# Kernel optimization log

Hardware: AMD Instinct MI355X
Metric: run time of the kernel (lower is better)

## Reference

```python
import jax, jax.numpy as jnp
import numpy as np

B, S, D, H = 4, 2048, 1024, 16
HD = D // H  # head_dim = 64

def setup_inputs() -> dict:
    key = jax.random.key(0)
    ks = jax.random.split(key, 11)
    s = 1.0 / np.sqrt(D)
    return {
        "query": jax.random.normal(ks[0], (B, S, D), jnp.float32),
        "key": jax.random.normal(ks[1], (B, S, D), jnp.float32),
        "value": jax.random.normal(ks[2], (B, S, D), jnp.float32),
        "Wq": jax.random.normal(ks[3], (D, D), jnp.float32) * s,
        "bq": jnp.zeros((D,), jnp.float32),
        "Wk": jax.random.normal(ks[4], (D, D), jnp.float32) * s,
        "bk": jnp.zeros((D,), jnp.float32),
        "Wv": jax.random.normal(ks[5], (D, D), jnp.float32) * s,
        "bv": jnp.zeros((D,), jnp.float32),
        "Wo": jax.random.normal(ks[6], (D, D), jnp.float32) * s,
        "bo": jnp.zeros((D,), jnp.float32),
    }

def reference(query, key, value, Wq, bq, Wk, bk, Wv, bv, Wo, bo):
    b = query.shape[0]
    # linear projections, then split heads -> [b, H, S, HD]
    Q = (query @ Wq + bq).reshape(b, -1, H, HD).transpose(0, 2, 1, 3)
    K = (key @ Wk + bk).reshape(b, -1, H, HD).transpose(0, 2, 1, 3)
    V = (value @ Wv + bv).reshape(b, -1, H, HD).transpose(0, 2, 1, 3)
    energy = jnp.einsum('bhqd,bhkd->bhqk', Q, K) / np.sqrt(HD)  # [b,H,S,S]
    attn = jax.nn.softmax(energy, axis=-1)
    x = jnp.einsum('bhqk,bhkd->bhqd', attn, V)
    x = x.transpose(0, 2, 1, 3).reshape(b, -1, H * HD)
    return x @ Wo + bo
```

## Files before the change

### kernel.cpp

```cpp
#include <hip/hip_runtime.h>
#include <math.h>

constexpr int Bb = 4, Ss = 2048, Dd = 1024, Hh = 16, HDd = 64;

typedef __attribute__((ext_vector_type(8))) short short8;
typedef __attribute__((ext_vector_type(4))) float floatx4;
typedef __attribute__((ext_vector_type(16))) float floatx16;
typedef __attribute__((ext_vector_type(4))) unsigned int uint4v;

__device__ inline unsigned short bf16r(float f) {
    unsigned int u = __builtin_bit_cast(unsigned int, f);
    u += 0x7fffu + ((u >> 16) & 1u);
    return (unsigned short)(u >> 16);
}
__device__ inline unsigned int cvtpk(float lo, float hi) {
    unsigned int r;
    asm("v_cvt_pk_bf16_f32 %0, %1, %2" : "=v"(r) : "v"(lo), "v"(hi));
    return r;
}

__device__ inline void gld16(const void* g, void* l) {
    __builtin_amdgcn_global_load_lds((const __attribute__((address_space(1))) void*)g,
                                     (__attribute__((address_space(3))) void*)l, 16, 0, 0);
}

__device__ inline floatx4 mfma16(short8 a, short8 b, floatx4 c) {
    return __builtin_amdgcn_mfma_f32_16x16x32_bf16(a, b, c, 0, 0, 0);
}
__device__ inline floatx16 mfma32(short8 a, short8 b, floatx16 c) {
    return __builtin_amdgcn_mfma_f32_32x32x16_bf16(a, b, c, 0, 0, 0);
}

#define LOG2E 1.4426950408889634f
#define EXP2_SHIFT 17.312340490667562f

__global__ __launch_bounds__(256)
void conv_w_kernel(const float* __restrict__ Wq, const float* __restrict__ Wk,
                   const float* __restrict__ Wv, const float* __restrict__ Wo,
                   unsigned short* __restrict__ Wt)
{
    int z = blockIdx.z;
    const float* W = z == 0 ? Wq : z == 1 ? Wk : z == 2 ? Wv : Wo;
    float scale = z == 0 ? 0.125f * LOG2E : 1.0f;
    unsigned short* out = Wt + (size_t)z * 1024 * 1024;

    int r0 = blockIdx.x * 64;
    int c0 = blockIdx.y * 64;
    int t = threadIdx.x;
    int oc = (t & 3) * 16;
    int orow = c0 + (t >> 2);

    float v[16];
    #pragma unroll
    for (int j = 0; j < 16; ++j)
        v[j] = W[(size_t)(r0 + oc + j) * 1024 + orow] * scale;

    unsigned int pk[8];
    #pragma unroll
    for (int j = 0; j < 8; ++j) pk[j] = cvtpk(v[2 * j], v[2 * j + 1]);

    uint4v w0 = {pk[0], pk[1], pk[2], pk[3]};
    uint4v w1 = {pk[4], pk[5], pk[6], pk[7]};
    *(uint4v*)(out + (size_t)orow * 1024 + r0 + oc) = w0;
    *(uint4v*)(out + (size_t)orow * 1024 + r0 + oc + 8) = w1;
}

__global__ __launch_bounds__(256)
void conv_bias_kernel(const float* __restrict__ bq, float* __restrict__ bqs)
{
    int idx = blockIdx.x * 256 + threadIdx.x;
    if (idx < 1024) bqs[idx] = bq[idx] * 0.125f * LOG2E;
}

__global__ __launch_bounds__(256)
void qkv_gemm_kernel(const float* __restrict__ qin, const float* __restrict__ kin,
                     const float* __restrict__ vin,
                     const unsigned short* __restrict__ Wt,
                     const float* __restrict__ bqs, const float* __restrict__ bk,
                     const float* __restrict__ bv,
                     unsigned short* __restrict__ Qb, unsigned short* __restrict__ Kb,
                     unsigned short* __restrict__ Vb)
{
    int z = blockIdx.z;
    const float* A = z == 0 ? qin : z == 1 ? kin : vin;
    const unsigned short* W = Wt + (size_t)z * 1048576;
    const float* bias = z == 0 ? bqs : z == 1 ? bk : bv;
    unsigned short* O = z == 0 ? Qb : z == 1 ? Kb : Vb;

    __shared__ __align__(16) char qsm[65536];
    char* Aa0 = qsm;
    char* Aa1 = qsm + 16384;
    char* Aa2 = qsm + 32768;
    char* Bb0 = qsm + 49152;
    char* Bb1 = qsm + 57344;

    int tid = threadIdx.x, lane = tid & 63, w = tid >> 6;
    int wr = w >> 1, wc = w & 1;
    int fr = lane & 15, fg = lane >> 4;
    int m0 = blockIdx.x * 128, n0 = blockIdx.y * 128;

    int arow_base = w * 32 + (lane >> 3);
    int asrc_col = (((lane & 7) ^ ((lane >> 3) & 7)) << 4) >> 2;
    const int bRdoB = ((wc * 64 + fr) * 32 + fg * 8) * 2;

    floatx4 acc[4][4] = {};

#define ISSUEA(kt, dst) {                                                       \
    _Pragma("unroll")                                                           \
    for (int j_ = 0; j_ < 4; ++j_) {                                            \
        const float* g_ = A + (size_t)(m0 + arow_base + j_ * 8) * 1024          \
                            + (kt) * 32 + asrc_col;                             \
        gld16(g_, (dst) + (size_t)((w << 8) + (j_ << 6) + lane) * 16);          \
    }}
#define GLB(kt, dst) {                                                          \
    const unsigned short* g0_ = W + (size_t)(n0 + (tid >> 2)) * 1024 + (kt) * 32 + (tid & 3) * 8;          \
    gld16(g0_, (dst) + (size_t)(w * 64) * 16);                                  \
    const unsigned short* g1_ = W + (size_t)(n0 + ((tid + 256) >> 2)) * 1024 + (kt) * 32 + (tid & 3) * 8;  \
    gld16(g1_, (dst) + (size_t)(256 + w * 64) * 16); }
#define COMP(Ac, Bc) { short8 af_[4], bf_[4];                                   \
    _Pragma("unroll")                                                           \
    for (int mi = 0; mi < 4; ++mi) {                                            \
        int row_ = wr * 64 + mi * 16 + fr;                                      \
        int xb_ = (row_ & 7) << 4;                                              \
        floatx4 al_ = *(const floatx4*)((Ac) + row_ * 128 + ((fg * 32) ^ xb_)); \
        floatx4 ah_ = *(const floatx4*)((Ac) + row_ * 128 + ((fg * 32 + 16) ^ xb_)); \
        uint4v u_ = {cvtpk(al_[0], al_[1]), cvtpk(al_[2], al_[3]),              \
                     cvtpk(ah_[0], ah_[1]), cvtpk(ah_[2], ah_[3])};             \
        af_[mi] = __builtin_bit_cast(short8, u_);                               \
    }                                                                           \
    _Pragma("unroll")                                                           \
    for (int ni = 0; ni < 4; ++ni) bf_[ni] = *(const short8*)((Bc) + bRdoB + ni * 1024); \
    _Pragma("unroll")                                                           \
    for (int mi = 0; mi < 4; ++mi)                                              \
        _Pragma("unroll")                                                       \
        for (int ni = 0; ni < 4; ++ni)                                          \
            acc[mi][ni] = mfma16(af_[mi], bf_[ni], acc[mi][ni]); }
#define FV10 { asm volatile("s_waitcnt vmcnt(10)" ::: "memory");                \
    __builtin_amdgcn_s_barrier(); __builtin_amdgcn_sched_barrier(0); }
#define FV6  { asm volatile("s_waitcnt vmcnt(6)" ::: "memory");                 \
    __builtin_amdgcn_s_barrier(); __builtin_amdgcn_sched_barrier(0); }
#define FV0  { asm volatile("s_waitcnt vmcnt(0)" ::: "memory");                 \
    __builtin_amdgcn_s_barrier(); __builtin_amdgcn_sched_barrier(0); }
#define FL   { asm volatile("s_waitcnt lgkmcnt(0)" ::: "memory");               \
    __builtin_amdgcn_s_barrier(); __builtin_amdgcn_sched_barrier(0); }

    ISSUEA(0, Aa0); GLB(0, Bb0); ISSUEA(1, Aa1);

    for (int p = 0; p < 5; ++p) {
        int kt = 6 * p;
        GLB(kt + 1, Bb1); ISSUEA(kt + 2, Aa2); FV10; COMP(Aa0, Bb0); FL;
        GLB(kt + 2, Bb0); ISSUEA(kt + 3, Aa0); FV10; COMP(Aa1, Bb1); FL;
        GLB(kt + 3, Bb1); ISSUEA(kt + 4, Aa1); FV10; COMP(Aa2, Bb0); FL;
        GLB(kt + 4, Bb0); ISSUEA(kt + 5, Aa2); FV10; COMP(Aa0, Bb1); FL;
        GLB(kt + 5, Bb1); ISSUEA(kt + 6, Aa0); FV10; COMP(Aa1, Bb0); FL;
        GLB(kt + 6, Bb0); ISSUEA(kt + 7, Aa1); FV10; COMP(Aa2, Bb1); FL;
    }

    GLB(31, Bb1);
    FV6; COMP(Aa0, Bb0); FL;
    FV0; COMP(Aa1, Bb1);
    __syncthreads();

#undef ISSUEA
#undef GLB
#undef COMP
#undef FV10
#undef FV6
#undef FV0
#undef FL

    float bvv[4];
    #pragma unroll
    for (int ni = 0; ni < 4; ++ni) bvv[ni] = bias[n0 + wc * 64 + ni * 16 + fr];

    if (z == 2) {
        unsigned short* T = (unsigned short*)(qsm) + (size_t)w * 4608;
        #pragma unroll
        for (int mi = 0; mi < 4; ++mi)
            #pragma unroll
            for (int ni = 0; ni < 4; ++ni) {
                int hdl = ni * 16 + fr;
                int sl  = mi * 16 + fg * 4;
                uint2 u2;
                u2.x = cvtpk(acc[mi][ni][0] + bvv[ni], acc[mi][ni][1] + bvv[ni]);
                u2.y = cvtpk(acc[mi][ni][2] + bvv[ni], acc[mi][ni][3] + bvv[ni]);
                *(uint2*)(T + hdl * 72 + sl) = u2;
            }
        __syncthreads();
        int h  = (n0 + wc * 64) >> 6;
        int Ms = m0 + wr * 64;
        int b_ = Ms >> 11, sbase = Ms & 2047;
        unsigned short* Od = O + (((size_t)(b_ * 16 + h) * 64) << 11) + sbase;
        int rg = lane >> 3, sc = lane & 7;
        #pragma unroll
        for (int j = 0; j < 8; ++j) {
            int row = j * 8 + rg;
            uint4v t = *(const uint4v*)(T + row * 72 + sc * 8);
            *(uint4v*)(Od + ((size_t)row << 11) + sc * 8) = t;
        }
    } else {
        #pragma unroll
        for (int mi = 0; mi < 4; ++mi)
            #pragma unroll
            for (int ni = 0; ni < 4; ++ni) {
                int n = n0 + wc * 64 + ni * 16 + fr;
                int h = n >> 6, hd = n & 63;
                #pragma unroll
                for (int i = 0; i < 4; ++i) {
                    int m = m0 + wr * 64 + mi * 16 + fg * 4 + i;
                    int b_ = m >> 11, s = m & 2047;
                    float val = acc[mi][ni][i] + bvv[ni];
                    O[(((size_t)(b_ * 16 + h) * 2048 + s) << 6) + hd] = bf16r(val);
                }
            }
    }
}

__global__ __launch_bounds__(256)
void attn_kernel(const unsigned short* __restrict__ Qb, const unsigned short* __restrict__ Kb,
                 const unsigned short* __restrict__ Vtb, unsigned short* __restrict__ Xb)
{
    __shared__ __align__(16) char smem[32768];

    int pphys = blockIdx.x + (blockIdx.y << 4) + (blockIdx.z << 8);
    int L = (pphys & 7) * 128 + (pphys >> 3);
    int qt = L & 15;
    int h  = (L >> 4) & 15;
    int b  = L >> 8;

    int tid = threadIdx.x, lane = tid & 63, w = tid >> 6;
    int c = lane & 31, hi = lane >> 5;
    int q0 = qt * 128;
    size_t base = ((size_t)(b * 16 + h)) * 2048 * 64;
    const unsigned short* Qp = Qb + base + (size_t)(q0 + w * 32) * 64;
    const unsigned short* Kp = Kb + base;
    const unsigned short* Vp = Vtb + base;

    short8 qfr[4];
    #pragma unroll
    for (int ks = 0; ks < 4; ++ks)
        qfr[ks] = *(const short8*)(Qp + (size_t)c * 64 + ks * 16 + hi * 8);

    floatx16 acc_o[2] = {};
    floatx16 acc_l = {};
    uint4v onesu = {0x3F803F80u, 0x3F803F80u, 0x3F803F80u, 0x3F803F80u};
    short8 onesb = __builtin_bit_cast(short8, onesu);

    int p0 = tid & 7;
    int r0 = tid >> 3;
    int r1 = r0 + 32;
    int g0 = p0 ^ (r0 & 7);

    auto STAGE = [&](int kt, char* Kd, char* Vd) {
        gld16(Kp + ((size_t)(kt * 64 + r0) << 6) + g0 * 8, Kd + (size_t)tid * 16);
        gld16(Kp + ((size_t)(kt * 64 + r1) << 6) + g0 * 8, Kd + (size_t)(tid + 256) * 16);
        gld16(Vp + ((size_t)r0 << 11) + kt * 64 + g0 * 8, Vd + (size_t)tid * 16);
        gld16(Vp + ((size_t)r1 << 11) + kt * 64 + g0 * 8, Vd + (size_t)(tid + 256) * 16);
    };

    STAGE(0, smem, smem + 8192);
    __syncthreads();

    for (int kt = 0; kt < 32; ++kt) {
        char* Kl = smem + (kt & 1) * 16384;
        char* Vl = Kl + 8192;
        if (kt + 1 < 32) {
            char* Kn = smem + ((kt + 1) & 1) * 16384;
            STAGE(kt + 1, Kn, Kn + 8192);
        }

        #pragma unroll
        for (int kvt = 0; kvt < 2; ++kvt) {
            floatx16 st;
            #pragma unroll
            for (int r = 0; r < 16; ++r) st[r] = -EXP2_SHIFT;

            __builtin_amdgcn_s_setprio(1);
            #pragma unroll
            for (int ks = 0; ks < 4; ++ks) {
                int row = kvt * 32 + c;
                short8 kf = *(const short8*)(Kl + row * 128 +
                                             ((ks * 32 + hi * 16) ^ ((row & 7) << 4)));
                st = mfma32(kf, qfr[ks], st);
            }
            __builtin_amdgcn_s_setprio(0);

            float p[16];
            #pragma unroll
            for (int r = 0; r < 16; ++r)
                p[r] = __builtin_amdgcn_exp2f(st[r]);
            unsigned int j[8];
            #pragma unroll
            for (int t2 = 0; t2 < 8; ++t2)
                j[t2] = cvtpk(p[2 * t2], p[2 * t2 + 1]);
            asm volatile("v_permlane32_swap_b32 %0, %1" : "+v"(j[0]), "+v"(j[2]));
            asm volatile("v_permlane32_swap_b32 %0, %1" : "+v"(j[1]), "+v"(j[3]));
            asm volatile("v_permlane32_swap_b32 %0, %1" : "+v"(j[4]), "+v"(j[6]));
            asm volatile("v_permlane32_swap_b32 %0, %1" : "+v"(j[5]), "+v"(j[7]));
            uint4v pa0 = {j[0], j[1], j[2], j[3]};
            uint4v pa1 = {j[4], j[5], j[6], j[7]};
            short8 paA = __builtin_bit_cast(short8, pa0);
            short8 paB = __builtin_bit_cast(short8, pa1);

            __builtin_amdgcn_s_setprio(1);
            #pragma unroll
            for (int kvs2 = 0; kvs2 < 2; ++kvs2) {
                int kstep = kvt * 2 + kvs2;
                short8 pa = kvs2 ? paB : paA;
                #pragma unroll
                for (int dvt = 0; dvt < 2; ++dvt) {
                    int dv = dvt * 32 + c;
                    short8 vf = *(const short8*)(Vl + dv * 128 +
                                                 ((kstep * 32 + hi * 16) ^ ((dv & 7) << 4)));
                    acc_o[dvt] = mfma32(pa, vf, acc_o[dvt]);
                }
            }
            acc_l = mfma32(paA, onesb, acc_l);
            acc_l = mfma32(paB, onesb, acc_l);
            __builtin_amdgcn_s_setprio(0);
        }
        __syncthreads();
    }

    unsigned short* Ot = (unsigned short*)smem;

    #pragma unroll
    for (int r = 0; r < 16; ++r) {
        int rowq = (r & 3) + 8 * (r >> 2) + 4 * hi;
        float inv = 1.0f / acc_l[r];
        int ql = w * 32 + rowq;
        Ot[ql * 64 + c]      = bf16r(acc_o[0][r] * inv);
        Ot[ql * 64 + 32 + c] = bf16r(acc_o[1][r] * inv);
    }
    __syncthreads();

    {
        int row = tid >> 1, half = tid & 1;
        const unsigned short* src = Ot + row * 64 + half * 32;
        unsigned short* dst = Xb + ((size_t)b * 2048 + q0 + row) * 1024
                                 + h * 64 + half * 32;
        uint4v v0 = *(const uint4v*)(src);
        uint4v v1 = *(const uint4v*)(src + 8);
        uint4v v2 = *(const uint4v*)(src + 16);
        uint4v v3 = *(const uint4v*)(src + 24);
        *(uint4v*)(dst) = v0;
        *(uint4v*)(dst + 8) = v1;
        *(uint4v*)(dst + 16) = v2;
        *(uint4v*)(dst + 24) = v3;
    }
}

__global__ __launch_bounds__(256)
void out_gemm_kernel(const unsigned short* __restrict__ Xb,
                     const unsigned short* __restrict__ Wto,
                     const float* __restrict__ bo, float* __restrict__ out)
{
    __shared__ __align__(16) char osm[32768];
    unsigned short* Asm0 = (unsigned short*)(osm);
    unsigned short* Bsm0 = (unsigned short*)(osm + 8192);
    unsigned short* Asm1 = (unsigned short*)(osm + 16384);
    unsigned short* Bsm1 = (unsigned short*)(osm + 24576);

    int tid = threadIdx.x, lane = tid & 63, w = tid >> 6;
    int wr = w >> 1, wc = w & 1;
    int fr = lane & 15, fg = lane >> 4;
    int m0 = blockIdx.x * 128, n0 = blockIdx.y * 128;

    const int aRdo = (wr * 64 + fr) * 32 + fg * 8;
    const int bRdo = (wc * 64 + fr) * 32 + fg * 8;

    floatx4 acc[4][4] = {};

    auto STAGE = [&](int k0, unsigned short* Ad, unsigned short* Bd) {
        #pragma unroll
        for (int it = 0; it < 2; ++it) {
            int cA = tid + it * 256;
            const unsigned short* ga = Xb + (size_t)(m0 + (cA >> 2)) * 1024 + k0 + (cA & 3) * 8;
            gld16(ga, (char*)Ad + (size_t)(it * 256 + w * 64) * 16);
            const unsigned short* gb = Wto + (size_t)(n0 + (cA >> 2)) * 1024 + k0 + (cA & 3) * 8;
            gld16(gb, (char*)Bd + (size_t)(it * 256 + w * 64) * 16);
        }
    };

    STAGE(0, Asm0, Bsm0);
    __syncthreads();

    for (int kt = 0; kt < 32; ++kt) {
        unsigned short* Acur = (kt & 1) ? Asm1 : Asm0;
        unsigned short* Bcur = (kt & 1) ? Bsm1 : Bsm0;
        if (kt < 31)
            STAGE((kt + 1) * 32, (kt & 1) ? Asm0 : Asm1, (kt & 1) ? Bsm0 : Bsm1);

        short8 af[4], bf[4];
        #pragma unroll
        for (int mi = 0; mi < 4; ++mi) af[mi] = *(const short8*)(Acur + aRdo + mi * 16 * 32);
        #pragma unroll
        for (int ni = 0; ni < 4; ++ni) bf[ni] = *(const short8*)(Bcur + bRdo + ni * 16 * 32);
        #pragma unroll
        for (int mi = 0; mi < 4; ++mi)
            #pragma unroll
            for (int ni = 0; ni < 4; ++ni)
                acc[mi][ni] = mfma16(af[mi], bf[ni], acc[mi][ni]);
        __syncthreads();
    }

    float bvv[4];
    #pragma unroll
    for (int ni = 0; ni < 4; ++ni) bvv[ni] = bo[n0 + wc * 64 + ni * 16 + fr];

    #pragma unroll
    for (int mi = 0; mi < 4; ++mi)
        #pragma unroll
        for (int ni = 0; ni < 4; ++ni) {
            int n = n0 + wc * 64 + ni * 16 + fr;
            #pragma unroll
            for (int i = 0; i < 4; ++i) {
                int m = m0 + wr * 64 + mi * 16 + fg * 4 + i;
                out[(size_t)m * 1024 + n] = acc[mi][ni][i] + bvv[ni];
            }
        }
}

extern "C" void kernel_launch(void* const* d_in, const int* in_sizes, int n_in,
                              void* d_out, int out_size, void* d_ws, size_t ws_size,
                              hipStream_t stream)
{
    const float* qin = (const float*)d_in[0];
    const float* kin = (const float*)d_in[1];
    const float* vin = (const float*)d_in[2];
    const float* Wq  = (const float*)d_in[3];
    const float* bq  = (const float*)d_in[4];
    const float* Wk  = (const float*)d_in[5];
    const float* bk  = (const float*)d_in[6];
    const float* Wv  = (const float*)d_in[7];
    const float* bv  = (const float*)d_in[8];
    const float* Wo  = (const float*)d_in[9];
    const float* bo  = (const float*)d_in[10];
    float* out = (float*)d_out;

    char* ws = (char*)d_ws;
    unsigned short* Wt  = (unsigned short*)(ws);
    float*          bqs = (float*)(ws + 8388608);
    unsigned short* Qb  = (unsigned short*)(ws + 8392704);
    unsigned short* Kb  = (unsigned short*)(ws + 8392704 + 16777216);
    unsigned short* Vb  = (unsigned short*)(ws + 8392704 + 2 * 16777216);
    unsigned short* Xb  = (unsigned short*)(ws + 8392704 + 3 * 16777216);

    conv_w_kernel<<<dim3(16, 16, 4), 256, 0, stream>>>(Wq, Wk, Wv, Wo, Wt);
    conv_bias_kernel<<<dim3(4), 256, 0, stream>>>(bq, bqs);
    qkv_gemm_kernel<<<dim3(64, 8, 3), 256, 0, stream>>>(qin, kin, vin, Wt, bqs, bk, bv,
                                                        Qb, Kb, Vb);
    attn_kernel<<<dim3(16, 16, 4), 256, 0, stream>>>(Qb, Kb, Vb, Xb);
    out_gemm_kernel<<<dim3(64, 8), 256, 0, stream>>>(Xb, Wt + 3145728, bo, out);
}
```

Measured before the change: 205.2 us.

## Load QKV GEMM weight fragments directly into registers instead of LDS

The QKV projection GEMM now reads bf16 weight fragments straight from global memory into per-lane registers (double-buffered even/odd sets) instead of staging them through LDS. This removes the B-tile LDS region, its LDS reads and one barrier per k-step, and shrinks shared memory from 64KB to 48KB, which may allow more blocks per CU. In exchange it raises register pressure, and the per-lane 16-byte global loads are strided across rows, so they may coalesce less well than the old LDS-staged path.

```diff
diff --git a/kernel.cpp b/kernel.cpp
--- a/kernel.cpp
+++ b/kernel.cpp
@@ -87,12 +87,10 @@
     const float* bias = z == 0 ? bqs : z == 1 ? bk : bv;
     unsigned short* O = z == 0 ? Qb : z == 1 ? Kb : Vb;
 
-    __shared__ __align__(16) char qsm[65536];
+    __shared__ __align__(16) char qsm[49152];
     char* Aa0 = qsm;
     char* Aa1 = qsm + 16384;
     char* Aa2 = qsm + 32768;
-    char* Bb0 = qsm + 49152;
-    char* Bb1 = qsm + 57344;
 
     int tid = threadIdx.x, lane = tid & 63, w = tid >> 6;
     int wr = w >> 1, wc = w & 1;
@@ -101,9 +99,11 @@
 
     int arow_base = w * 32 + (lane >> 3);
     int asrc_col = (((lane & 7) ^ ((lane >> 3) & 7)) << 4) >> 2;
-    const int bRdoB = ((wc * 64 + fr) * 32 + fg * 8) * 2;
+
+    const unsigned short* Wfrag = W + (size_t)(n0 + wc * 64 + fr) * 1024 + fg * 8;
 
     floatx4 acc[4][4] = {};
+    uint4v bE[4], bO[4];
 
 #define ISSUEA(kt, dst) {                                                       \
     _Pragma("unroll")                                                           \
@@ -112,12 +112,11 @@
                             + (kt) * 32 + asrc_col;                             \
         gld16(g_, (dst) + (size_t)((w << 8) + (j_ << 6) + lane) * 16);          \
     }}
-#define GLB(kt, dst) {                                                          \
-    const unsigned short* g0_ = W + (size_t)(n0 + (tid >> 2)) * 1024 + (kt) * 32 + (tid & 3) * 8;          \
-    gld16(g0_, (dst) + (size_t)(w * 64) * 16);                                  \
-    const unsigned short* g1_ = W + (size_t)(n0 + ((tid + 256) >> 2)) * 1024 + (kt) * 32 + (tid & 3) * 8;  \
-    gld16(g1_, (dst) + (size_t)(256 + w * 64) * 16); }
-#define COMP(Ac, Bc) { short8 af_[4], bf_[4];                                   \
+#define ISSUEB(kt, br) {                                                        \
+    _Pragma("unroll")                                                           \
+    for (int ni_ = 0; ni_ < 4; ++ni_)                                           \
+        br[ni_] = *(const uint4v*)(Wfrag + (size_t)(ni_ * 16) * 1024 + (kt) * 32); }
+#define COMP(Ac, br) { short8 af_[4], bf_[4];                                   \
     _Pragma("unroll")                                                           \
     for (int mi = 0; mi < 4; ++mi) {                                            \
         int row_ = wr * 64 + mi * 16 + fr;                                      \
@@ -129,45 +128,38 @@
         af_[mi] = __builtin_bit_cast(short8, u_);                               \
     }                                                                           \
     _Pragma("unroll")                                                           \
-    for (int ni = 0; ni < 4; ++ni) bf_[ni] = *(const short8*)((Bc) + bRdoB + ni * 1024); \
+    for (int ni = 0; ni < 4; ++ni) bf_[ni] = __builtin_bit_cast(short8, br[ni]); \
     _Pragma("unroll")                                                           \
     for (int mi = 0; mi < 4; ++mi)                                              \
         _Pragma("unroll")                                                       \
         for (int ni = 0; ni < 4; ++ni)                                          \
             acc[mi][ni] = mfma16(af_[mi], bf_[ni], acc[mi][ni]); }
-#define FV10 { asm volatile("s_waitcnt vmcnt(10)" ::: "memory");                \
+#define FV8  { asm volatile("s_waitcnt vmcnt(8) lgkmcnt(0)" ::: "memory");      \
     __builtin_amdgcn_s_barrier(); __builtin_amdgcn_sched_barrier(0); }
-#define FV6  { asm volatile("s_waitcnt vmcnt(6)" ::: "memory");                 \
+#define FV0  { asm volatile("s_waitcnt vmcnt(0) lgkmcnt(0)" ::: "memory");      \
     __builtin_amdgcn_s_barrier(); __builtin_amdgcn_sched_barrier(0); }
-#define FV0  { asm volatile("s_waitcnt vmcnt(0)" ::: "memory");                 \
-    __builtin_amdgcn_s_barrier(); __builtin_amdgcn_sched_barrier(0); }
-#define FL   { asm volatile("s_waitcnt lgkmcnt(0)" ::: "memory");               \
-    __builtin_amdgcn_s_barrier(); __builtin_amdgcn_sched_barrier(0); }
-
-    ISSUEA(0, Aa0); GLB(0, Bb0); ISSUEA(1, Aa1);
+
+    ISSUEB(0, bE); ISSUEA(0, Aa0); ISSUEB(1, bO); ISSUEA(1, Aa1);
 
     for (int p = 0; p < 5; ++p) {
         int kt = 6 * p;
-        GLB(kt + 1, Bb1); ISSUEA(kt + 2, Aa2); FV10; COMP(Aa0, Bb0); FL;
-        GLB(kt + 2, Bb0); ISSUEA(kt + 3, Aa0); FV10; COMP(Aa1, Bb1); FL;
-        GLB(kt + 3, Bb1); ISSUEA(kt + 4, Aa1); FV10; COMP(Aa2, Bb0); FL;
-        GLB(kt + 4, Bb0); ISSUEA(kt + 5, Aa2); FV10; COMP(Aa0, Bb1); FL;
-        GLB(kt + 5, Bb1); ISSUEA(kt + 6, Aa0); FV10; COMP(Aa1, Bb0); FL;
-        GLB(kt + 6, Bb0); ISSUEA(kt + 7, Aa1); FV10; COMP(Aa2, Bb1); FL;
-    }
-
-    GLB(31, Bb1);
-    FV6; COMP(Aa0, Bb0); FL;
-    FV0; COMP(Aa1, Bb1);
+        FV8; COMP(Aa0, bE); ISSUEB(kt + 2, bE); ISSUEA(kt + 2, Aa2);
+        FV8; COMP(Aa1, bO); ISSUEB(kt + 3, bO); ISSUEA(kt + 3, Aa0);
+        FV8; COMP(Aa2, bE); ISSUEB(kt + 4, bE); ISSUEA(kt + 4, Aa1);
+        FV8; COMP(Aa0, bO); ISSUEB(kt + 5, bO); ISSUEA(kt + 5, Aa2);
+        FV8; COMP(Aa1, bE); ISSUEB(kt + 6, bE); ISSUEA(kt + 6, Aa0);
+        FV8; COMP(Aa2, bO); ISSUEB(kt + 7, bO); ISSUEA(kt + 7, Aa1);
+    }
+
+    FV8; COMP(Aa0, bE);
+    FV0; COMP(Aa1, bO);
     __syncthreads();
 
 #undef ISSUEA
-#undef GLB
+#undef ISSUEB
 #undef COMP
-#undef FV10
-#undef FV6
+#undef FV8
 #undef FV0
-#undef FL
 
     float bvv[4];
     #pragma unroll
```

Result: slower. 248.0 us (+20.9%).
